# Kernel tuning notes

Hardware: AMD Instinct MI355X
Metric: run time of the kernel (lower is better)

Reference implementation:

```python
import jax, jax.numpy as jnp
import numpy as np

SOM = (32, 32)   # som_dim; SOM[0]*SOM[1] == num_embeddings
LR = 0.05


def setup_inputs() -> dict:
    key = jax.random.key(0)
    k1, k2 = jax.random.split(key)
    B, K, D = 65536, 1024, 256
    x = jax.random.normal(k1, (B, D), dtype=jnp.float32)
    embeddings = jax.random.uniform(k2, (K, D), dtype=jnp.float32)  # torch.rand init
    return {"x": x, "embeddings": embeddings}


def reference(x, embeddings):
    K, D = embeddings.shape
    # pairwise squared distances: [B, K]
    dist = (jnp.sum(x * x, axis=1, keepdims=True)
            + jnp.sum(embeddings * embeddings, axis=1)
            - 2.0 * (x @ embeddings.T))
    n_min = jnp.argmin(dist, axis=1)          # [B]
    z_q = embeddings[n_min]                   # [B, D]

    # SOM grid coordinates and clamped neighbors
    n_x = n_min // SOM[1]
    n_y = n_min % SOM[1]
    x_up = jnp.where(n_x < SOM[0] - 1, n_x + 1, n_x)
    x_down = jnp.where(n_x > 0, n_x - 1, n_x)
    y_right = jnp.where(n_y < SOM[1] - 1, n_y + 1, n_y)
    y_left = jnp.where(n_y > 0, n_y - 1, n_y)
    idx_up = x_up * SOM[1] + n_y
    idx_down = x_down * SOM[1] + n_y
    idx_right = n_x * SOM[1] + y_right
    idx_left = n_x * SOM[1] + y_left

    # [B, 4, D] neighbor gather (order: up, down, left, right as in torch code)
    nbr_idx = jnp.stack([idx_up, idx_down, idx_left, idx_right], axis=1)
    z_q_neighbors = embeddings[nbr_idx]

    # SOM scatter update (torch does one-hot matmuls; segment_sum is the fused form)
    dw = x - z_q                              # [B, D]
    seg = lambda idx: jax.ops.segment_sum(dw, idx, num_segments=K)
    new_embeddings = jax.lax.stop_gradient(
        embeddings
        + LR * seg(n_min)
        + 0.5 * LR * (seg(idx_up) + seg(idx_down) + seg(idx_right) + seg(idx_left))
    )

    commit_loss = jnp.mean((x - z_q) ** 2)
    som_loss = jnp.mean((jax.lax.stop_gradient(x)[:, None, :] - z_q_neighbors) ** 2)
    return z_q, commit_loss, som_loss, new_embeddings
```

## Files before the change

### kernel.cpp

```cpp
#include <hip/hip_runtime.h>

#define B_ROWS 65536
#define DDIM   256
#define KEMB   1024
#define LRC    0.05f
#define BM 64
#define BN 128

typedef __attribute__((ext_vector_type(8))) _Float16 half8;
typedef __attribute__((ext_vector_type(4))) float f32x4;

#define SX_OFF    0u
#define CNT_OFF   1048576u
#define SUMS_OFF  1052672u
#define ESQ_OFF   1053312u
#define CUR_OFF   1057408u
#define NMIN_OFF  1061504u
#define ROWS_OFF  1585792u
#define EH_OFF    1847936u

static __device__ __forceinline__ unsigned short f2h(float f) {
  _Float16 h = (_Float16)f;
  return *(unsigned short*)&h;
}
static __device__ __forceinline__ float h2f(unsigned short u) {
  _Float16 h = *(_Float16*)&u;
  return (float)h;
}

__global__ __launch_bounds__(256) void convert_kernel(
    const float* __restrict__ E, unsigned short* __restrict__ Eh,
    float* __restrict__ esq) {
  size_t i = (size_t)blockIdx.x * 256 + threadIdx.x;
  size_t off = i * 8;
  const float4 v0 = *(const float4*)(E + off);
  const float4 v1 = *(const float4*)(E + off + 4);
  float f[8] = {v0.x, v0.y, v0.z, v0.w, v1.x, v1.y, v1.z, v1.w};
  unsigned short h[8];
  float part = 0.f;
#pragma unroll
  for (int j = 0; j < 8; ++j) {
    h[j] = f2h(f[j]);
    part += f[j] * f[j];
  }
  *(uint4*)(Eh + off) = *(const uint4*)h;
  float s = part;
  for (int o = 16; o > 0; o >>= 1) s += __shfl_down(s, o, 32);
  if ((threadIdx.x & 31) == 0) esq[i >> 5] = s;
}

__global__ __launch_bounds__(256, 2) void gemm_argmin_kernel(
    const float* __restrict__ X, const unsigned short* __restrict__ EhW,
    const float* __restrict__ esq, const float* __restrict__ Ef,
    int* __restrict__ nmin, int* __restrict__ counts, float* __restrict__ zq,
    double* __restrict__ sums) {
  __shared__ __align__(16) unsigned short sX[2][8][256][8];

  const int tid  = threadIdx.x;
  const int lane = tid & 63, w = tid >> 6;
  const int lrow = lane & 15;
  const int qidx = lane >> 4;
  const int rowbase = (w >> 1) * 32;
  const int colb    = (w & 1) * 64;
  const int bm0 = (int)blockIdx.x * BM;

  {
    const int row = tid >> 2, p = tid & 3;
    const float* xp = X + (size_t)(bm0 + row) * DDIM + p * 64;
    float part = 0.f;
#pragma unroll
    for (int j = 0; j < 8; ++j) {
      const float4 a = *(const float4*)(xp + j * 8);
      const float4 b = *(const float4*)(xp + j * 8 + 4);
      float f[8] = {a.x, a.y, a.z, a.w, b.x, b.y, b.z, b.w};
      unsigned short hh[8], ll[8];
#pragma unroll
      for (int m = 0; m < 8; ++m) {
        hh[m] = f2h(f[m]);
        ll[m] = f2h(f[m] - h2f(hh[m]));
        part += f[m] * f[m];
      }
      const int kcc = p * 2 + (j >> 2);
      const int ch  = (row << 2) | ((j & 3) ^ ((row >> 1) & 3));
      *(uint4*)&sX[0][kcc][ch][0] = *(const uint4*)hh;
      *(uint4*)&sX[1][kcc][ch][0] = *(const uint4*)ll;
    }
#pragma unroll
    for (int o = 32; o > 0; o >>= 1) part += __shfl_down(part, o);
    if (lane == 0)
      atomicAdd(&sums[8 + (((int)blockIdx.x * 4 + w) & 63)], (double)part);
  }

  float rbest[8];
  int   ridx[8];
#pragma unroll
  for (int i = 0; i < 8; ++i) { rbest[i] = 3.4e38f; ridx[i] = 0; }

  int ra[2];
#pragma unroll
  for (int t = 0; t < 2; ++t) {
    const int m = rowbase + t * 16 + lrow;
    ra[t] = (m << 2) | (qidx ^ ((m >> 1) & 3));
  }
  const unsigned short* bp[4];
#pragma unroll
  for (int t = 0; t < 4; ++t)
    bp[t] = EhW + (size_t)(colb + t * 16 + lrow) * DDIM + qidx * 8;

  __syncthreads();

  for (int nt = 0; nt < 8; ++nt) {
    f32x4 acc[2][4];
#pragma unroll
    for (int i = 0; i < 2; ++i)
#pragma unroll
      for (int j = 0; j < 4; ++j) acc[i][j] = (f32x4){0.f, 0.f, 0.f, 0.f};

    const size_t ntoff = (size_t)nt * BN * DDIM;
#pragma unroll
    for (int kcc = 0; kcc < 8; ++kcc) {
      half8 af0[2], af1[2], bfr[4];
#pragma unroll
      for (int t = 0; t < 4; ++t)
        bfr[t] = *(const half8*)(bp[t] + ntoff + kcc * 32);
#pragma unroll
      for (int t = 0; t < 2; ++t) {
        af0[t] = *(const half8*)&sX[0][kcc][ra[t]][0];
        af1[t] = *(const half8*)&sX[1][kcc][ra[t]][0];
      }
#pragma unroll
      for (int tr = 0; tr < 2; ++tr)
#pragma unroll
        for (int tc = 0; tc < 4; ++tc)
          acc[tr][tc] = __builtin_amdgcn_mfma_f32_16x16x32_f16(
              af0[tr], bfr[tc], acc[tr][tc], 0, 0, 0);
#pragma unroll
      for (int tr = 0; tr < 2; ++tr)
#pragma unroll
        for (int tc = 0; tc < 4; ++tc)
          acc[tr][tc] = __builtin_amdgcn_mfma_f32_16x16x32_f16(
              af1[tr], bfr[tc], acc[tr][tc], 0, 0, 0);
    }
#pragma unroll
    for (int tc = 0; tc < 4; ++tc) {
      const int col = nt * BN + colb + tc * 16 + lrow;
      const float eq = esq[col];
#pragma unroll
      for (int tr = 0; tr < 2; ++tr)
#pragma unroll
        for (int rr = 0; rr < 4; ++rr) {
          float d = eq - 2.0f * acc[tr][tc][rr];
          const int slot = tr * 4 + rr;
          if (d < rbest[slot]) { rbest[slot] = d; ridx[slot] = col; }
        }
    }
  }

  __syncthreads();
  float* cdd = (float*)&sX[0][0][0][0];
  int*   cdi = (int*)(cdd + 128);
  int*   snm = cdi + 128;
  int*   h   = snm + 64;

#pragma unroll
  for (int i = 0; i < 4; ++i) h[tid + i * 256] = 0;

#pragma unroll
  for (int slot = 0; slot < 8; ++slot) {
    float bd = rbest[slot];
    int   bi = ridx[slot];
#pragma unroll
    for (int off = 1; off < 16; off <<= 1) {
      float od = __shfl_xor(bd, off, 64);
      int   oi = __shfl_xor(bi, off, 64);
      if (od < bd || (od == bd && oi < bi)) { bd = od; bi = oi; }
    }
    if (lrow == 0) {
      const int row = rowbase + (slot >> 2) * 16 + (lane >> 4) * 4 + (slot & 3);
      cdd[(w & 1) * 64 + row] = bd;
      cdi[(w & 1) * 64 + row] = bi;
    }
  }
  __syncthreads();
  if (tid < BM) {
    float d0 = cdd[tid], d1 = cdd[64 + tid];
    int   i0 = cdi[tid], i1 = cdi[64 + tid];
    int bi = (d1 < d0 || (d1 == d0 && i1 < i0)) ? i1 : i0;
    nmin[bm0 + tid] = bi;
    snm[tid] = bi;
    atomicAdd(&h[bi], 1);
  }
  __syncthreads();
#pragma unroll
  for (int i = 0; i < 4; ++i) {
    int v = h[tid + i * 256];
    if (v) atomicAdd(&counts[tid + i * 256], v);
  }
  const int r0 = w * 16;
#pragma unroll 4
  for (int r = 0; r < 16; ++r) {
    const int k = snm[r0 + r];
    const float4 v = *(const float4*)(Ef + (size_t)k * DDIM + lane * 4);
    *(float4*)(zq + (size_t)(bm0 + r0 + r) * DDIM + lane * 4) = v;
  }
}

__global__ __launch_bounds__(1024) void scan_kernel(
    const int* __restrict__ counts, int* __restrict__ cur) {
  __shared__ int tmp[KEMB];
  int tid = threadIdx.x;
  int v = counts[tid];
  tmp[tid] = v;
  __syncthreads();
  for (int off = 1; off < 1024; off <<= 1) {
    int u = (tid >= off) ? tmp[tid - off] : 0;
    __syncthreads();
    tmp[tid] += u;
    __syncthreads();
  }
  cur[tid] = tmp[tid] - v;
}

__global__ __launch_bounds__(1024) void scatter_kernel(
    const int* __restrict__ nm, int* __restrict__ cur,
    int* __restrict__ rows) {
  __shared__ int lcnt[KEMB], lbase[KEMB], lrank[KEMB];
  int tid = threadIdx.x;
  lcnt[tid] = 0; lrank[tid] = 0;
  __syncthreads();
  int b = blockIdx.x * 1024 + tid;
  int k = nm[b];
  atomicAdd(&lcnt[k], 1);
  __syncthreads();
  if (lcnt[tid] > 0) lbase[tid] = atomicAdd(&cur[tid], lcnt[tid]);
  __syncthreads();
  int r = atomicAdd(&lrank[k], 1);
  rows[lbase[k] + r] = b;
}

__global__ __launch_bounds__(256) void sxsum_kernel(
    const int* __restrict__ rows, const int* __restrict__ nm,
    const float* __restrict__ X, float* __restrict__ SX) {
  __shared__ int sb[32], sk[32];
  int tid = threadIdx.x;
  int p0 = blockIdx.x * 32;
  if (tid < 32) sb[tid] = rows[p0 + tid];
  __syncthreads();
  if (tid < 32) sk[tid] = nm[sb[tid]];
  __syncthreads();
  float acc = 0.f;
  int kprev = sk[0];
  for (int i = 0; i < 32; ++i) {
    int k = sk[i];
    if (k != kprev) {
      atomicAdd(&SX[(size_t)kprev * DDIM + tid], acc);
      acc = 0.f;
      kprev = k;
    }
    acc += X[(size_t)sb[i] * DDIM + tid];
  }
  atomicAdd(&SX[(size_t)kprev * DDIM + tid], acc);
}

__global__ __launch_bounds__(256) void stencil_kernel(
    const float* __restrict__ E, const float* __restrict__ SX,
    const int* __restrict__ counts, const float* __restrict__ esq,
    double* __restrict__ sums, float* __restrict__ out) {
  __shared__ float redc[256], reds[256];
  int k = blockIdx.x, t = threadIdx.x;
  int kx = k >> 5, ky = k & 31;
  int j1 = (kx >= 1)  ? k - 32 : k;
  int j2 = (kx <= 30) ? k + 32 : k;
  int j3 = (ky >= 1)  ? k - 1  : k;
  int j4 = (ky <= 30) ? k + 1  : k;
  int fU = (kx < 31) ? k + 32 : k;
  int fD = (kx > 0)  ? k - 32 : k;
  int fL = (ky > 0)  ? k - 1  : k;
  int fR = (ky < 31) ? k + 1  : k;

  float e   = E[(size_t)k * DDIM + t];
  float sxk = SX[(size_t)k * DDIM + t];
  float Tk = sxk - (float)counts[k] * e;
  float T1 = SX[(size_t)j1 * DDIM + t] - (float)counts[j1] * E[(size_t)j1 * DDIM + t];
  float T2 = SX[(size_t)j2 * DDIM + t] - (float)counts[j2] * E[(size_t)j2 * DDIM + t];
  float T3 = SX[(size_t)j3 * DDIM + t] - (float)counts[j3] * E[(size_t)j3 * DDIM + t];
  float T4 = SX[(size_t)j4 * DDIM + t] - (float)counts[j4] * E[(size_t)j4 * DDIM + t];
  float v = e + LRC * Tk + 0.5f * LRC * (T1 + T2 + T3 + T4);
  out[(size_t)B_ROWS * DDIM + 2 + (size_t)k * DDIM + t] = v;

  float eU = E[(size_t)fU * DDIM + t], eD = E[(size_t)fD * DDIM + t];
  float eL = E[(size_t)fL * DDIM + t], eR = E[(size_t)fR * DDIM + t];
  float cp = -2.f * sxk * e;
  float sp = -2.f * sxk * (eU + eD + eL + eR);
  if (t == 0) {
    float ck = (float)counts[k];
    cp += ck * esq[k];
    sp += ck * (esq[fU] + esq[fD] + esq[fL] + esq[fR]);
  }
  redc[t] = cp; reds[t] = sp;
  __syncthreads();
  for (int s = 128; s > 0; s >>= 1) {
    if (t < s) { redc[t] += redc[t + s]; reds[t] += reds[t + s]; }
    __syncthreads();
  }
  if (t == 0) {
    atomicAdd(&sums[1], (double)redc[0]);
    atomicAdd(&sums[2], (double)reds[0]);
  }
}

__global__ void finalize_kernel(const double* __restrict__ sums,
                                float* __restrict__ out) {
  double xsq = 0.0;
  for (int s = 0; s < 64; ++s) xsq += sums[8 + s];
  out[(size_t)B_ROWS * DDIM]     = (float)((xsq + sums[1]) / ((double)B_ROWS * DDIM));
  out[(size_t)B_ROWS * DDIM + 1] =
      (float)((4.0 * xsq + sums[2]) / ((double)B_ROWS * 4.0 * DDIM));
}

extern "C" void kernel_launch(void* const* d_in, const int* in_sizes, int n_in,
                              void* d_out, int out_size, void* d_ws, size_t ws_size,
                              hipStream_t stream) {
  const float* X = (const float*)d_in[0];
  const float* E = (const float*)d_in[1];
  float* out = (float*)d_out;
  char* ws = (char*)d_ws;

  float*          SX   = (float*)(ws + SX_OFF);
  int*            cnts = (int*)(ws + CNT_OFF);
  double*         sums = (double*)(ws + SUMS_OFF);
  float*          esq  = (float*)(ws + ESQ_OFF);
  int*            cur  = (int*)(ws + CUR_OFF);
  int*            nm   = (int*)(ws + NMIN_OFF);
  int*            rows = (int*)(ws + ROWS_OFF);
  unsigned short* EhW  = (unsigned short*)(ws + EH_OFF);

  hipMemsetAsync(ws, 0, ESQ_OFF, stream);

  convert_kernel<<<KEMB * (DDIM / 8) / 256, 256, 0, stream>>>(E, EhW, esq);
  gemm_argmin_kernel<<<B_ROWS / BM, 256, 0, stream>>>(X, EhW, esq, E, nm, cnts, out,
                                                      sums);
  scan_kernel<<<1, 1024, 0, stream>>>(cnts, cur);
  scatter_kernel<<<B_ROWS / 1024, 1024, 0, stream>>>(nm, cur, rows);
  sxsum_kernel<<<B_ROWS / 32, 256, 0, stream>>>(rows, nm, X, SX);
  stencil_kernel<<<KEMB, 256, 0, stream>>>(E, SX, cnts, esq, sums, out);
  finalize_kernel<<<1, 1, 0, stream>>>(sums, out);
}
```

Baseline: 298.7 us.

## Stage embedding tiles into LDS via async global_load_lds double buffering

The embedding B-operand is no longer read straight from global memory into registers for each MFMA k-step. Each k-chunk tile is now loaded with global_load_lds into a swizzled, double-buffered LDS array, and the next tile is prefetched while the current one is computed. The X staging loop is also reorganised so that consecutive threads write contiguous LDS chunks. The aim is to hide global-load latency and share each embedding tile across waves, at the cost of 16KB more LDS, which may lower occupancy, and a __syncthreads after every k-step.

```diff
diff --git a/kernel.cpp b/kernel.cpp
--- a/kernel.cpp
+++ b/kernel.cpp
@@ -26,6 +26,11 @@
 static __device__ __forceinline__ float h2f(unsigned short u) {
   _Float16 h = *(_Float16*)&u;
   return (float)h;
+}
+static __device__ __forceinline__ void glds16(const void* g, void* l) {
+  __builtin_amdgcn_global_load_lds(
+      (const __attribute__((address_space(1))) unsigned int*)g,
+      (__attribute__((address_space(3))) unsigned int*)l, 16, 0, 0);
 }
 
 __global__ __launch_bounds__(256) void convert_kernel(
@@ -55,6 +60,7 @@
     int* __restrict__ nmin, int* __restrict__ counts, float* __restrict__ zq,
     double* __restrict__ sums) {
   __shared__ __align__(16) unsigned short sX[2][8][256][8];
+  __shared__ __align__(16) unsigned short sE[2][512][8];
 
   const int tid  = threadIdx.x;
   const int lane = tid & 63, w = tid >> 6;
@@ -64,14 +70,30 @@
   const int colb    = (w & 1) * 64;
   const int bm0 = (int)blockIdx.x * BM;
 
+  int ec_row[2], ec_q8[2];
+#pragma unroll
+  for (int j = 0; j < 2; ++j) {
+    const int c = j * 256 + tid;
+    ec_row[j] = c >> 2;
+    ec_q8[j]  = ((c & 3) ^ ((ec_row[j] >> 1) & 3)) * 8;
+  }
+
+#pragma unroll
+  for (int j = 0; j < 2; ++j)
+    glds16(EhW + (size_t)ec_row[j] * DDIM + ec_q8[j], (char*)&sE[0][j * 256 + tid][0]);
+
   {
-    const int row = tid >> 2, p = tid & 3;
-    const float* xp = X + (size_t)(bm0 + row) * DDIM + p * 64;
     float part = 0.f;
 #pragma unroll
-    for (int j = 0; j < 8; ++j) {
-      const float4 a = *(const float4*)(xp + j * 8);
-      const float4 b = *(const float4*)(xp + j * 8 + 4);
+    for (int it = 0; it < 8; ++it) {
+      const int c   = it * 256 + tid;
+      const int kcc = c >> 8;
+      const int cc  = c & 255;
+      const int row = cc >> 2;
+      const int q   = (cc & 3) ^ ((row >> 1) & 3);
+      const float* xp = X + (size_t)(bm0 + row) * DDIM + kcc * 32 + q * 8;
+      const float4 a = *(const float4*)xp;
+      const float4 b = *(const float4*)(xp + 4);
       float f[8] = {a.x, a.y, a.z, a.w, b.x, b.y, b.z, b.w};
       unsigned short hh[8], ll[8];
 #pragma unroll
@@ -80,10 +102,8 @@
         ll[m] = f2h(f[m] - h2f(hh[m]));
         part += f[m] * f[m];
       }
-      const int kcc = p * 2 + (j >> 2);
-      const int ch  = (row << 2) | ((j & 3) ^ ((row >> 1) & 3));
-      *(uint4*)&sX[0][kcc][ch][0] = *(const uint4*)hh;
-      *(uint4*)&sX[1][kcc][ch][0] = *(const uint4*)ll;
+      *(uint4*)((char*)sX + (size_t)c * 16)          = *(const uint4*)hh;
+      *(uint4*)((char*)sX + (size_t)(c + 2048) * 16) = *(const uint4*)ll;
     }
 #pragma unroll
     for (int o = 32; o > 0; o >>= 1) part += __shfl_down(part, o);
@@ -96,16 +116,17 @@
 #pragma unroll
   for (int i = 0; i < 8; ++i) { rbest[i] = 3.4e38f; ridx[i] = 0; }
 
-  int ra[2];
+  int ra[2], rb[4];
 #pragma unroll
   for (int t = 0; t < 2; ++t) {
     const int m = rowbase + t * 16 + lrow;
     ra[t] = (m << 2) | (qidx ^ ((m >> 1) & 3));
   }
-  const unsigned short* bp[4];
-#pragma unroll
-  for (int t = 0; t < 4; ++t)
-    bp[t] = EhW + (size_t)(colb + t * 16 + lrow) * DDIM + qidx * 8;
+#pragma unroll
+  for (int t = 0; t < 4; ++t) {
+    const int n = colb + t * 16 + lrow;
+    rb[t] = (n << 2) | (qidx ^ ((n >> 1) & 3));
+  }
 
   __syncthreads();
 
@@ -116,19 +137,29 @@
 #pragma unroll
       for (int j = 0; j < 4; ++j) acc[i][j] = (f32x4){0.f, 0.f, 0.f, 0.f};
 
-    const size_t ntoff = (size_t)nt * BN * DDIM;
 #pragma unroll
     for (int kcc = 0; kcc < 8; ++kcc) {
+      const int s   = nt * 8 + kcc;
+      const int cur = s & 1;
+      if (s < 63) {
+        const int ns = s + 1;
+        const int nnt = ns >> 3, nk = ns & 7;
+#pragma unroll
+        for (int j = 0; j < 2; ++j) {
+          const int c = j * 256 + tid;
+          glds16(EhW + (size_t)(nnt * BN + ec_row[j]) * DDIM + nk * 32 + ec_q8[j],
+                 (char*)&sE[cur ^ 1][c][0]);
+        }
+      }
       half8 af0[2], af1[2], bfr[4];
-#pragma unroll
-      for (int t = 0; t < 4; ++t)
-        bfr[t] = *(const half8*)(bp[t] + ntoff + kcc * 32);
 #pragma unroll
       for (int t = 0; t < 2; ++t) {
         af0[t] = *(const half8*)&sX[0][kcc][ra[t]][0];
         af1[t] = *(const half8*)&sX[1][kcc][ra[t]][0];
       }
 #pragma unroll
+      for (int t = 0; t < 4; ++t) bfr[t] = *(const half8*)&sE[cur][rb[t]][0];
+#pragma unroll
       for (int tr = 0; tr < 2; ++tr)
 #pragma unroll
         for (int tc = 0; tc < 4; ++tc)
@@ -140,6 +171,7 @@
         for (int tc = 0; tc < 4; ++tc)
           acc[tr][tc] = __builtin_amdgcn_mfma_f32_16x16x32_f16(
               af1[tr], bfr[tc], acc[tr][tc], 0, 0, 0);
+      __syncthreads();
     }
 #pragma unroll
     for (int tc = 0; tc < 4; ++tc) {
@@ -156,11 +188,10 @@
     }
   }
 
-  __syncthreads();
-  float* cdd = (float*)&sX[0][0][0][0];
+  float* cdd = (float*)&sE[0][0][0];
   int*   cdi = (int*)(cdd + 128);
   int*   snm = cdi + 128;
-  int*   h   = snm + 64;
+  int*   h   = (int*)&sX[0][0][0][0];
 
 #pragma unroll
   for (int i = 0; i < 4; ++i) h[tid + i * 256] = 0;
```

Result: faster. 250.3 us (-16.2%).
